# Performance work log

Hardware: AMD Instinct MI355X
Metric: run time of the kernel (lower is better)

The kernel has to match this reference:

```python
import jax, jax.numpy as jnp
import numpy as np

B, S, H, NH = 8, 512, 4096, 64
HD = H // NH  # head dim = 64
LN_EPS = 1e-12
TOL_BITS = 16


def quant16(x):
    """Per-tensor dynamic fixed-point quantization to 16 bits.

    int_bit_width = ceil(log2(max|x|)) + 1 (sign bit); frac = 16 - int_bits.
    Values are rounded to the fixed-point grid and clipped to int16 range.
    """
    m = jnp.max(jnp.abs(x))
    int_bw = jnp.ceil(jnp.log2(jnp.maximum(m, 1e-12))) + 1.0
    frac_bw = jnp.asarray(TOL_BITS, x.dtype) - int_bw
    scale = jnp.exp2(frac_bw).astype(x.dtype)
    q = jnp.clip(jnp.round(x * scale), -32768.0, 32767.0) / scale
    return q


def setup_inputs() -> dict:
    key = jax.random.key(0)
    ks = jax.random.split(key, 6)
    s = 0.02
    return {
        "input_ids": jax.random.normal(ks[0], (B, S, H), jnp.float32),
        "attention_mask": jnp.zeros((B, 1, 1, S), jnp.float32),
        "Wq": jax.random.normal(ks[1], (H, H), jnp.float32) * s,
        "bq": jnp.zeros((H,), jnp.float32),
        "Wk": jax.random.normal(ks[2], (H, H), jnp.float32) * s,
        "bk": jnp.zeros((H,), jnp.float32),
        "Wv": jax.random.normal(ks[3], (H, H), jnp.float32) * s,
        "bv": jnp.zeros((H,), jnp.float32),
        "Wd": jax.random.normal(ks[4], (H, H), jnp.float32) * s,
        "bd": jnp.zeros((H,), jnp.float32),
        "ln_w": jnp.ones((H,), jnp.float32),
        "ln_b": jnp.zeros((H,), jnp.float32),
    }


def reference(input_ids, attention_mask, Wq, bq, Wk, bk, Wv, bv, Wd, bd, ln_w, ln_b):
    x = input_ids  # [B,S,H]
    # Q/K/V projections (torch Linear: y = x @ W.T + b), each followed by quant
    q = quant16(jnp.einsum('bsh,oh->bso', x, Wq) + bq)
    k = quant16(jnp.einsum('bsh,oh->bso', x, Wk) + bk)
    v = quant16(jnp.einsum('bsh,oh->bso', x, Wv) + bv)
    # split heads -> [B,NH,S,HD]
    q = q.reshape(B, S, NH, HD).transpose(0, 2, 1, 3)
    k = k.reshape(B, S, NH, HD).transpose(0, 2, 1, 3)
    v = v.reshape(B, S, NH, HD).transpose(0, 2, 1, 3)
    scores = jnp.einsum('bnqd,bnkd->bnqk', q, k) / np.sqrt(HD).astype(np.float32)
    scores = quant16(scores)
    scores = scores + attention_mask
    probs = jax.nn.softmax(scores, axis=-1)
    probs = quant16(probs)
    ctx = quant16(jnp.einsum('bnqk,bnkd->bnqd', probs, v))
    ctx = ctx.transpose(0, 2, 1, 3)  # [B,S,NH,HD]
    # dense: w = Wd.T reshaped to (NH, HD, H)
    w = Wd.T.reshape(NH, HD, H)
    proj = quant16(jnp.einsum('bfnd,ndh->bfh', ctx, w) + bd)
    # residual + LayerNorm
    y = x + proj
    mu = jnp.mean(y, axis=-1, keepdims=True)
    var = jnp.mean(jnp.square(y - mu), axis=-1, keepdims=True)
    y = (y - mu) / jnp.sqrt(var + LN_EPS) * ln_w + ln_b
    return quant16(y)
```

## Files before the change

kernel.cpp:

```cpp
#include <hip/hip_runtime.h>
#include <hip/hip_bf16.h>
#include <stdint.h>


typedef __attribute__((ext_vector_type(4))) float f32x4;
typedef __attribute__((ext_vector_type(8))) __bf16 bf16x8;

__device__ inline unsigned short f2bf(float f) {
  union { float f; unsigned u; } c; c.f = f;
  unsigned r = (c.u + 0x7fffu + ((c.u >> 16) & 1u)) >> 16;
  return (unsigned short)r;
}

__device__ inline void gload_lds16(const void* g, void* l) {
  __builtin_amdgcn_global_load_lds(
      (const __attribute__((address_space(1))) void*)g,
      (__attribute__((address_space(3))) void*)l, 16, 0, 0);
}

__global__ __launch_bounds__(256) void conv_all(
    const float* __restrict__ x, const float* __restrict__ wq,
    const float* __restrict__ wk, const float* __restrict__ wv,
    const float* __restrict__ wd, unsigned short* __restrict__ out) {
  int i = blockIdx.x * 256 + threadIdx.x;
  int reg = i >> 21;
  int off = i & 2097151;
  const float* src = (reg == 0) ? x : (reg == 1) ? wq : (reg == 2) ? wk
                     : (reg == 3) ? wv : wd;
  const float4* ip = (const float4*)src;
  float4 a = ip[off * 2], b = ip[off * 2 + 1];
  union { unsigned short s[8]; uint4 v; } o;
  o.s[0] = f2bf(a.x); o.s[1] = f2bf(a.y); o.s[2] = f2bf(a.z); o.s[3] = f2bf(a.w);
  o.s[4] = f2bf(b.x); o.s[5] = f2bf(b.y); o.s[6] = f2bf(b.z); o.s[7] = f2bf(b.w);
  ((uint4*)out)[i] = o.v;
}

template <int BIAS_MODE, int OUT_BF16>
__global__ __launch_bounds__(512, 2) void gemm_4p(
    const unsigned short* __restrict__ A, const unsigned short* __restrict__ Bw,
    const float* __restrict__ bias0, const float* __restrict__ bias1,
    const float* __restrict__ bias2, void* __restrict__ Cout,
    int M, int N, int K) {
  extern __shared__ unsigned short lds[];
  const int nbm = M >> 8, nbn = N >> 8, nwg = nbm * nbn;
  const int bid = blockIdx.x;
  const int wg = (bid & 7) * (nwg >> 3) + (bid >> 3);
  const int bm = wg % nbm, bn = wg / nbm;
  const int tid = threadIdx.x, w = tid >> 6, l = tid & 63;
  const int wr = w >> 2, wc = w & 3;
  const int lr = l & 15, lg = l >> 4;
  const unsigned short* gA = A + (size_t)bm * 256 * K;
  const unsigned short* gB = Bw + (size_t)bn * 256 * K;
  const int NT = K >> 6;
  const int srow = tid >> 3;
  const int scol = ((tid & 7) ^ (srow & 7)) << 3;
  f32x4 acc[8][4] = {};
  bf16x8 a[8], b[8];

#define STG(op, buf, h, kt)                                                    \
  {                                                                            \
    const unsigned short* g_ = (op) ? gB : gA;                                 \
    _Pragma("unroll")                                                          \
    for (int j_ = 0; j_ < 2; ++j_) {                                           \
      gload_lds16(                                                             \
          g_ + (size_t)((h) * 128 + j_ * 64 + srow) * K + (kt) * 64 + scol,    \
          &lds[((op) * 2 + (buf)) * 16384 + ((h) * 128 + j_ * 64) * 64 +       \
               w * 512]);                                                      \
    }                                                                          \
  }

#define RDA(buf, m, kk)                                                        \
  (*(const bf16x8*)&lds[(buf) * 16384 + (wr * 128 + (m) * 16 + lr) * 64 +      \
                        ((((kk) * 4 + lg) ^ (lr & 7)) << 3)])
#define RDB(buf, n, kk)                                                        \
  (*(const bf16x8*)&lds[(2 + (buf)) * 16384 + (wc * 64 + (n) * 16 + lr) * 64 + \
                        ((((kk) * 4 + lg) ^ (lr & 7)) << 3)])

#define LDA(buf, mh)                                                           \
  _Pragma("unroll")                                                            \
  for (int m_ = 0; m_ < 4; ++m_) {                                             \
    a[m_ * 2 + 0] = RDA(buf, (mh) * 4 + m_, 0);                                \
    a[m_ * 2 + 1] = RDA(buf, (mh) * 4 + m_, 1);                                \
  }
#define LDB(buf, nh)                                                           \
  _Pragma("unroll")                                                            \
  for (int n_ = 0; n_ < 2; ++n_) {                                             \
    b[((nh) * 2 + n_) * 2 + 0] = RDB(buf, (nh) * 2 + n_, 0);                   \
    b[((nh) * 2 + n_) * 2 + 1] = RDB(buf, (nh) * 2 + n_, 1);                   \
  }

#define MM(mbase, nbase)                                                       \
  __builtin_amdgcn_s_setprio(1);                                               \
  _Pragma("unroll")                                                            \
  for (int m_ = 0; m_ < 4; ++m_) {                                             \
    _Pragma("unroll")                                                          \
    for (int n_ = 0; n_ < 2; ++n_) {                                           \
      acc[(mbase) + m_][(nbase) + n_] =                                        \
          __builtin_amdgcn_mfma_f32_16x16x32_bf16(                             \
              a[m_ * 2], b[((nbase) + n_) * 2], acc[(mbase) + m_][(nbase) + n_],\
              0, 0, 0);                                                        \
      acc[(mbase) + m_][(nbase) + n_] =                                        \
          __builtin_amdgcn_mfma_f32_16x16x32_bf16(                             \
              a[m_ * 2 + 1], b[((nbase) + n_) * 2 + 1],                        \
              acc[(mbase) + m_][(nbase) + n_], 0, 0, 0);                       \
    }                                                                          \
  }                                                                            \
  __builtin_amdgcn_s_setprio(0);

#define BAR() __builtin_amdgcn_s_barrier()
#define VMW4() asm volatile("s_waitcnt vmcnt(4)" ::: "memory")
#define VMW0() asm volatile("s_waitcnt vmcnt(0)" ::: "memory")

  STG(0, 0, 0, 0); STG(0, 0, 1, 0); STG(1, 0, 0, 0); STG(1, 0, 1, 0);
  STG(1, 1, 0, 1); STG(1, 1, 1, 1);
  VMW4();
  BAR();

  const int NI = NT >> 1;
  for (int i = 0; i < NI; ++i) {
    const int t1 = 2 * i + 1, t2 = 2 * i + 2, t3 = 2 * i + 3;
    const bool s2 = t2 < NT, s3 = t3 < NT;
    LDA(0, 0); LDB(0, 0); LDB(0, 1);
    STG(0, 1, 0, t1); STG(0, 1, 1, t1);
    BAR();
    MM(0, 0); MM(0, 2);
    LDA(0, 1);
    if (s2) { STG(1, 0, 0, t2); STG(1, 0, 1, t2); VMW4(); } else VMW0();
    BAR();
    MM(4, 0); MM(4, 2);
    LDA(1, 0); LDB(1, 0); LDB(1, 1);
    if (s2) { STG(0, 0, 0, t2); STG(0, 0, 1, t2); }
    BAR();
    MM(0, 0); MM(0, 2);
    LDA(1, 1);
    if (s3) { STG(1, 1, 0, t3); STG(1, 1, 1, t3); VMW4(); }
    else if (s2) VMW0();
    BAR();
    MM(4, 0); MM(4, 2);
  }

#pragma unroll
  for (int n = 0; n < 4; ++n) {
    int col = bn * 256 + wc * 64 + n * 16 + lr;
    float bv = 0.f;
    if (BIAS_MODE == 1) bv = bias0[col];
    else if (BIAS_MODE == 2)
      bv = (col < 4096) ? bias0[col] : (col < 8192 ? bias1[col - 4096] : bias2[col - 8192]);
#pragma unroll
    for (int m = 0; m < 8; ++m) {
#pragma unroll
      for (int r = 0; r < 4; ++r) {
        int row = bm * 256 + wr * 128 + m * 16 + lg * 4 + r;
        float v = acc[m][n][r] + bv;
        if (OUT_BF16)
          ((unsigned short*)Cout)[(size_t)row * N + col] = f2bf(v);
        else
          ((float*)Cout)[(size_t)row * N + col] = v;
      }
    }
  }
#undef STG
#undef RDA
#undef RDB
#undef LDA
#undef LDB
#undef MM
#undef BAR
#undef VMW4
#undef VMW0
}

__global__ __launch_bounds__(512) void attn_kernel(
    const unsigned short* __restrict__ qkv, const float* __restrict__ mask,
    unsigned short* __restrict__ ctx) {
  extern __shared__ char smem[];
  unsigned short* Kt = (unsigned short*)smem;
  unsigned short* Vt = Kt + 512 * 64;
  unsigned short* Pb = Vt + 64 * 512;
  float* Mb = (float*)(Pb + 8 * 16 * 64);

  const int bid = blockIdx.x;
  const int b = bid >> 6, h = bid & 63;
  const int tid = threadIdx.x, w = tid >> 6, l = tid & 63;
  const size_t tokbase = (size_t)b * 512;

  Mb[tid < 512 ? tid : 0] = mask[b * 512 + (tid < 512 ? tid : 0)];
#pragma unroll
  for (int it = 0; it < 8; ++it) {
    int idx = it * 512 + tid;
    int row = idx >> 3, g = (idx & 7) << 3;
    const unsigned short* src = qkv + (tokbase + row) * 12288 + 4096 + h * 64 + g;
    uint4 v = *(const uint4*)src;
    *(uint4*)&Kt[row * 64 + (g ^ ((row & 7) << 3))] = v;
  }
#pragma unroll
  for (int it = 0; it < 8; ++it) {
    int idx = it * 512 + tid;
    int key = idx >> 3, g = (idx & 7) << 3;
    const unsigned short* src = qkv + (tokbase + key) * 12288 + 8192 + h * 64 + g;
    uint4 v = *(const uint4*)src;
    const unsigned short* e = (const unsigned short*)&v;
#pragma unroll
    for (int i = 0; i < 8; i++) {
      int d = g + i;
      Vt[d * 512 + (key ^ ((d & 7) << 3))] = e[i];
    }
  }
  __syncthreads();

  unsigned short* Pw = Pb + w * 16 * 64;
  const int lr = l & 15, lg = l >> 4;

  for (int c = 0; c < 4; ++c) {
    int q0 = w * 64 + c * 16;
    const unsigned short* qsrc = qkv + (tokbase + q0 + lr) * 12288 + h * 64 + lg * 8;
    bf16x8 qa0 = *(const bf16x8*)qsrc;
    bf16x8 qa1 = *(const bf16x8*)(qsrc + 32);
    f32x4 sc[32];
    f32x4 zero = {0.f, 0.f, 0.f, 0.f};
#pragma unroll
    for (int n = 0; n < 32; n++) {
      int key = n * 16 + lr;
      bf16x8 kb0 = *(const bf16x8*)&Kt[key * 64 + ((lg * 8) ^ ((key & 7) << 3))];
      bf16x8 kb1 = *(const bf16x8*)&Kt[key * 64 + ((32 + lg * 8) ^ ((key & 7) << 3))];
      f32x4 a = __builtin_amdgcn_mfma_f32_16x16x32_bf16(qa0, kb0, zero, 0, 0, 0);
      sc[n] = __builtin_amdgcn_mfma_f32_16x16x32_bf16(qa1, kb1, a, 0, 0, 0);
    }
    float rmax[4] = {-1e30f, -1e30f, -1e30f, -1e30f};
#pragma unroll
    for (int n = 0; n < 32; n++) {
      float mk = Mb[n * 16 + lr];
#pragma unroll
      for (int r = 0; r < 4; r++) {
        float s = sc[n][r] * 0.125f + mk;
        sc[n][r] = s;
        rmax[r] = fmaxf(rmax[r], s);
      }
    }
#pragma unroll
    for (int r = 0; r < 4; r++) {
      float m = rmax[r];
      m = fmaxf(m, __shfl_xor(m, 8)); m = fmaxf(m, __shfl_xor(m, 4));
      m = fmaxf(m, __shfl_xor(m, 2)); m = fmaxf(m, __shfl_xor(m, 1));
      rmax[r] = m;
    }
    float rsum[4] = {0.f, 0.f, 0.f, 0.f};
#pragma unroll
    for (int n = 0; n < 32; n++)
#pragma unroll
      for (int r = 0; r < 4; r++) {
        float p = __expf(sc[n][r] - rmax[r]);
        sc[n][r] = p;
        rsum[r] += p;
      }
#pragma unroll
    for (int r = 0; r < 4; r++) {
      float s = rsum[r];
      s += __shfl_xor(s, 8); s += __shfl_xor(s, 4);
      s += __shfl_xor(s, 2); s += __shfl_xor(s, 1);
      rsum[r] = s;
    }
    f32x4 cacc[4] = {};
#pragma unroll
    for (int kb = 0; kb < 8; ++kb) {
#pragma unroll
      for (int nn = 0; nn < 4; ++nn) {
        int colp = nn * 16 + lr;
#pragma unroll
        for (int r = 0; r < 4; r++) {
          int m = lg * 4 + r;
          Pw[m * 64 + (colp ^ ((m & 7) << 3))] = f2bf(sc[kb * 4 + nn][r]);
        }
      }
      bf16x8 pa0 = *(const bf16x8*)&Pw[lr * 64 + ((lg * 8) ^ ((lr & 7) << 3))];
      bf16x8 pa1 = *(const bf16x8*)&Pw[lr * 64 + ((32 + lg * 8) ^ ((lr & 7) << 3))];
#pragma unroll
      for (int dt = 0; dt < 4; ++dt) {
        int vr = dt * 16 + lr;
        int k0 = kb * 64 + lg * 8;
        bf16x8 vb0 = *(const bf16x8*)&Vt[vr * 512 + (k0 ^ ((vr & 7) << 3))];
        bf16x8 vb1 = *(const bf16x8*)&Vt[vr * 512 + ((k0 + 32) ^ ((vr & 7) << 3))];
        cacc[dt] = __builtin_amdgcn_mfma_f32_16x16x32_bf16(pa0, vb0, cacc[dt], 0, 0, 0);
        cacc[dt] = __builtin_amdgcn_mfma_f32_16x16x32_bf16(pa1, vb1, cacc[dt], 0, 0, 0);
      }
    }
#pragma unroll
    for (int dt = 0; dt < 4; ++dt)
#pragma unroll
      for (int r = 0; r < 4; r++) {
        int row = q0 + lg * 4 + r;
        float v = cacc[dt][r] / rsum[r];
        ctx[(tokbase + row) * 4096 + h * 64 + dt * 16 + lr] = f2bf(v);
      }
  }
}

__global__ __launch_bounds__(256) void ln_kernel(
    const float* __restrict__ x, float* __restrict__ io,
    const float* __restrict__ lnw, const float* __restrict__ lnb) {
  int t = blockIdx.x;
  const float4* xr = (const float4*)(x + (size_t)t * 4096);
  float4* pr = (float4*)(io + (size_t)t * 4096);
  float4 y[4];
  float sum = 0.f, sq = 0.f;
#pragma unroll
  for (int j = 0; j < 4; j++) {
    int i4 = j * 256 + threadIdx.x;
    float4 xv = xr[i4], pv = pr[i4];
    float4 yy;
    yy.x = xv.x + pv.x; yy.y = xv.y + pv.y; yy.z = xv.z + pv.z; yy.w = xv.w + pv.w;
    sum += yy.x + yy.y + yy.z + yy.w;
    sq += yy.x * yy.x + yy.y * yy.y + yy.z * yy.z + yy.w * yy.w;
    y[j] = yy;
  }
#pragma unroll
  for (int off = 32; off >= 1; off >>= 1) {
    sum += __shfl_down(sum, off);
    sq += __shfl_down(sq, off);
  }
  __shared__ float red[8];
  int w = threadIdx.x >> 6, l = threadIdx.x & 63;
  if (l == 0) { red[w] = sum; red[4 + w] = sq; }
  __syncthreads();
  float ts = red[0] + red[1] + red[2] + red[3];
  float tq = red[4] + red[5] + red[6] + red[7];
  float mean = ts * (1.f / 4096.f);
  float var = tq * (1.f / 4096.f) - mean * mean;
  float rs = rsqrtf(var + 1e-12f);
#pragma unroll
  for (int j = 0; j < 4; j++) {
    int i4 = j * 256 + threadIdx.x;
    float4 wv = ((const float4*)lnw)[i4];
    float4 bb = ((const float4*)lnb)[i4];
    float4 o;
    o.x = (y[j].x - mean) * rs * wv.x + bb.x;
    o.y = (y[j].y - mean) * rs * wv.y + bb.y;
    o.z = (y[j].z - mean) * rs * wv.z + bb.z;
    o.w = (y[j].w - mean) * rs * wv.w + bb.w;
    pr[i4] = o;
  }
}

extern "C" void kernel_launch(void* const* d_in, const int* in_sizes, int n_in,
                              void* d_out, int out_size, void* d_ws, size_t ws_size,
                              hipStream_t stream) {
  const float* x   = (const float*)d_in[0];
  const float* msk = (const float*)d_in[1];
  const float* Wq  = (const float*)d_in[2];
  const float* bq  = (const float*)d_in[3];
  const float* Wk  = (const float*)d_in[4];
  const float* bk  = (const float*)d_in[5];
  const float* Wv  = (const float*)d_in[6];
  const float* bv  = (const float*)d_in[7];
  const float* Wd  = (const float*)d_in[8];
  const float* bd  = (const float*)d_in[9];
  const float* lnw = (const float*)d_in[10];
  const float* lnb = (const float*)d_in[11];
  float* out = (float*)d_out;

  unsigned short* xb    = (unsigned short*)d_ws;
  unsigned short* wqkvb = xb + (size_t)16777216;
  unsigned short* wdb   = wqkvb + (size_t)50331648;
  unsigned short* qkvb  = wdb + (size_t)16777216;
  unsigned short* ctxb  = wqkvb;

  conv_all<<<40960, 256, 0, stream>>>(x, Wq, Wk, Wv, Wd, xb);

  (void)hipFuncSetAttribute((const void*)(gemm_4p<2, 1>),
                            hipFuncAttributeMaxDynamicSharedMemorySize, 131072);
  (void)hipFuncSetAttribute((const void*)(gemm_4p<1, 0>),
                            hipFuncAttributeMaxDynamicSharedMemorySize, 131072);

  gemm_4p<2, 1><<<768, 512, 131072, stream>>>(xb, wqkvb, bq, bk, bv, qkvb,
                                              4096, 12288, 4096);

  (void)hipFuncSetAttribute((const void*)attn_kernel,
                            hipFuncAttributeMaxDynamicSharedMemorySize, 149504);
  attn_kernel<<<512, 512, 149504, stream>>>(qkvb, msk, ctxb);

  gemm_4p<1, 0><<<256, 512, 131072, stream>>>(ctxb, wdb, bd, nullptr, nullptr,
                                              out, 4096, 4096, 4096);

  ln_kernel<<<4096, 256, 0, stream>>>(x, out, lnw, lnb);
}
```

Before: 740.6 us.

## Shrink GEMM tiles to 128x128 with 4 waves per workgroup

The bf16 GEMM now uses 128x128 output tiles computed by 256 threads (4 waves in a 2x2 grid), where before it used 256x256 tiles with 512 threads. LDS per block drops from 128KB to 64KB and the grids grow to 3072 and 1024 workgroups. The aim is better wave coverage across the CUs, most of all for the output-projection GEMM, which before launched only 256 blocks. The cost is lower arithmetic intensity per tile and more global and L2 traffic, since each operand tile is reloaded more often.

New measurement: 864.3 us. 16.7% more time.

```diff
diff --git a/kernel.cpp b/kernel.cpp
--- a/kernel.cpp
+++ b/kernel.cpp
@@ -36,26 +36,26 @@
 }
 
 template <int BIAS_MODE, int OUT_BF16>
-__global__ __launch_bounds__(512, 2) void gemm_4p(
+__global__ __launch_bounds__(256, 2) void gemm_4p(
     const unsigned short* __restrict__ A, const unsigned short* __restrict__ Bw,
     const float* __restrict__ bias0, const float* __restrict__ bias1,
     const float* __restrict__ bias2, void* __restrict__ Cout,
     int M, int N, int K) {
   extern __shared__ unsigned short lds[];
-  const int nbm = M >> 8, nbn = N >> 8, nwg = nbm * nbn;
+  const int nbm = M >> 7, nbn = N >> 7, nwg = nbm * nbn;
   const int bid = blockIdx.x;
   const int wg = (bid & 7) * (nwg >> 3) + (bid >> 3);
   const int bm = wg % nbm, bn = wg / nbm;
   const int tid = threadIdx.x, w = tid >> 6, l = tid & 63;
-  const int wr = w >> 2, wc = w & 3;
+  const int wr = w >> 1, wc = w & 1;
   const int lr = l & 15, lg = l >> 4;
-  const unsigned short* gA = A + (size_t)bm * 256 * K;
-  const unsigned short* gB = Bw + (size_t)bn * 256 * K;
+  const unsigned short* gA = A + (size_t)bm * 128 * K;
+  const unsigned short* gB = Bw + (size_t)bn * 128 * K;
   const int NT = K >> 6;
   const int srow = tid >> 3;
   const int scol = ((tid & 7) ^ (srow & 7)) << 3;
-  f32x4 acc[8][4] = {};
-  bf16x8 a[8], b[8];
+  f32x4 acc[4][4] = {};
+  bf16x8 a[4], b[8];
 
 #define STG(op, buf, h, kt)                                                    \
   {                                                                            \
@@ -63,46 +63,42 @@
     _Pragma("unroll")                                                          \
     for (int j_ = 0; j_ < 2; ++j_) {                                           \
       gload_lds16(                                                             \
-          g_ + (size_t)((h) * 128 + j_ * 64 + srow) * K + (kt) * 64 + scol,    \
-          &lds[((op) * 2 + (buf)) * 16384 + ((h) * 128 + j_ * 64) * 64 +       \
-               w * 512]);                                                      \
+          g_ + (size_t)((h) * 64 + j_ * 32 + srow) * K + (kt) * 64 + scol,     \
+          &lds[((op) * 2 + (buf)) * 8192 + ((h) * 64 + j_ * 32) * 64 +         \
+               tid * 8]);                                                      \
     }                                                                          \
   }
 
 #define RDA(buf, m, kk)                                                        \
-  (*(const bf16x8*)&lds[(buf) * 16384 + (wr * 128 + (m) * 16 + lr) * 64 +      \
+  (*(const bf16x8*)&lds[(buf) * 8192 + (wr * 64 + (m) * 16 + lr) * 64 +        \
                         ((((kk) * 4 + lg) ^ (lr & 7)) << 3)])
 #define RDB(buf, n, kk)                                                        \
-  (*(const bf16x8*)&lds[(2 + (buf)) * 16384 + (wc * 64 + (n) * 16 + lr) * 64 + \
+  (*(const bf16x8*)&lds[(2 + (buf)) * 8192 + (wc * 64 + (n) * 16 + lr) * 64 +  \
                         ((((kk) * 4 + lg) ^ (lr & 7)) << 3)])
 
 #define LDA(buf, mh)                                                           \
   _Pragma("unroll")                                                            \
-  for (int m_ = 0; m_ < 4; ++m_) {                                             \
-    a[m_ * 2 + 0] = RDA(buf, (mh) * 4 + m_, 0);                                \
-    a[m_ * 2 + 1] = RDA(buf, (mh) * 4 + m_, 1);                                \
-  }
-#define LDB(buf, nh)                                                           \
+  for (int m_ = 0; m_ < 2; ++m_) {                                             \
+    a[m_ * 2 + 0] = RDA(buf, (mh) * 2 + m_, 0);                                \
+    a[m_ * 2 + 1] = RDA(buf, (mh) * 2 + m_, 1);                                \
+  }
+#define LDB(buf)                                                               \
   _Pragma("unroll")                                                            \
-  for (int n_ = 0; n_ < 2; ++n_) {                                             \
-    b[((nh) * 2 + n_) * 2 + 0] = RDB(buf, (nh) * 2 + n_, 0);                   \
-    b[((nh) * 2 + n_) * 2 + 1] = RDB(buf, (nh) * 2 + n_, 1);                   \
-  }
-
-#define MM(mbase, nbase)                                                       \
+  for (int n_ = 0; n_ < 4; ++n_) {                                             \
+    b[n_ * 2 + 0] = RDB(buf, n_, 0);                                           \
+    b[n_ * 2 + 1] = RDB(buf, n_, 1);                                           \
+  }
+
+#define MM(mbase)                                                              \
   __builtin_amdgcn_s_setprio(1);                                               \
   _Pragma("unroll")                                                            \
-  for (int m_ = 0; m_ < 4; ++m_) {                                             \
+  for (int m_ = 0; m_ < 2; ++m_) {                                             \
     _Pragma("unroll")                                                          \
-    for (int n_ = 0; n_ < 2; ++n_) {                                           \
-      acc[(mbase) + m_][(nbase) + n_] =                                        \
-          __builtin_amdgcn_mfma_f32_16x16x32_bf16(                             \
-              a[m_ * 2], b[((nbase) + n_) * 2], acc[(mbase) + m_][(nbase) + n_],\
-              0, 0, 0);                                                        \
-      acc[(mbase) + m_][(nbase) + n_] =                                        \
-          __builtin_amdgcn_mfma_f32_16x16x32_bf16(                             \
-              a[m_ * 2 + 1], b[((nbase) + n_) * 2 + 1],                        \
-              acc[(mbase) + m_][(nbase) + n_], 0, 0, 0);                       \
+    for (int n_ = 0; n_ < 4; ++n_) {                                           \
+      acc[(mbase) + m_][n_] = __builtin_amdgcn_mfma_f32_16x16x32_bf16(         \
+          a[m_ * 2], b[n_ * 2], acc[(mbase) + m_][n_], 0, 0, 0);               \
+      acc[(mbase) + m_][n_] = __builtin_amdgcn_mfma_f32_16x16x32_bf16(         \
+          a[m_ * 2 + 1], b[n_ * 2 + 1], acc[(mbase) + m_][n_], 0, 0, 0);       \
     }                                                                          \
   }                                                                            \
   __builtin_amdgcn_s_setprio(0);
@@ -120,37 +116,37 @@
   for (int i = 0; i < NI; ++i) {
     const int t1 = 2 * i + 1, t2 = 2 * i + 2, t3 = 2 * i + 3;
     const bool s2 = t2 < NT, s3 = t3 < NT;
-    LDA(0, 0); LDB(0, 0); LDB(0, 1);
+    LDA(0, 0); LDB(0);
     STG(0, 1, 0, t1); STG(0, 1, 1, t1);
     BAR();
-    MM(0, 0); MM(0, 2);
+    MM(0);
     LDA(0, 1);
     if (s2) { STG(1, 0, 0, t2); STG(1, 0, 1, t2); VMW4(); } else VMW0();
     BAR();
-    MM(4, 0); MM(4, 2);
-    LDA(1, 0); LDB(1, 0); LDB(1, 1);
+    MM(2);
+    LDA(1, 0); LDB(1);
     if (s2) { STG(0, 0, 0, t2); STG(0, 0, 1, t2); }
     BAR();
-    MM(0, 0); MM(0, 2);
+    MM(0);
     LDA(1, 1);
     if (s3) { STG(1, 1, 0, t3); STG(1, 1, 1, t3); VMW4(); }
     else if (s2) VMW0();
     BAR();
-    MM(4, 0); MM(4, 2);
+    MM(2);
   }
 
 #pragma unroll
   for (int n = 0; n < 4; ++n) {
-    int col = bn * 256 + wc * 64 + n * 16 + lr;
+    int col = bn * 128 + wc * 64 + n * 16 + lr;
     float bv = 0.f;
     if (BIAS_MODE == 1) bv = bias0[col];
     else if (BIAS_MODE == 2)
       bv = (col < 4096) ? bias0[col] : (col < 8192 ? bias1[col - 4096] : bias2[col - 8192]);
 #pragma unroll
-    for (int m = 0; m < 8; ++m) {
+    for (int m = 0; m < 4; ++m) {
 #pragma unroll
       for (int r = 0; r < 4; ++r) {
-        int row = bm * 256 + wr * 128 + m * 16 + lg * 4 + r;
+        int row = bm * 128 + wr * 64 + m * 16 + lg * 4 + r;
         float v = acc[m][n][r] + bv;
         if (OUT_BF16)
           ((unsigned short*)Cout)[(size_t)row * N + col] = f2bf(v);
@@ -367,18 +363,18 @@
   conv_all<<<40960, 256, 0, stream>>>(x, Wq, Wk, Wv, Wd, xb);
 
   (void)hipFuncSetAttribute((const void*)(gemm_4p<2, 1>),
-                            hipFuncAttributeMaxDynamicSharedMemorySize, 131072);
+                            hipFuncAttributeMaxDynamicSharedMemorySize, 65536);
   (void)hipFuncSetAttribute((const void*)(gemm_4p<1, 0>),
-                            hipFuncAttributeMaxDynamicSharedMemorySize, 131072);
-
-  gemm_4p<2, 1><<<768, 512, 131072, stream>>>(xb, wqkvb, bq, bk, bv, qkvb,
+                            hipFuncAttributeMaxDynamicSharedMemorySize, 65536);
+
+  gemm_4p<2, 1><<<3072, 256, 65536, stream>>>(xb, wqkvb, bq, bk, bv, qkvb,
                                               4096, 12288, 4096);
 
   (void)hipFuncSetAttribute((const void*)attn_kernel,
                             hipFuncAttributeMaxDynamicSharedMemorySize, 149504);
   attn_kernel<<<512, 512, 149504, stream>>>(qkvb, msk, ctxb);
 
-  gemm_4p<1, 0><<<256, 512, 131072, stream>>>(ctxb, wdb, bd, nullptr, nullptr,
+  gemm_4p<1, 0><<<1024, 256, 65536, stream>>>(ctxb, wdb, bd, nullptr, nullptr,
                                               out, 4096, 4096, 4096);
 
   ln_kernel<<<4096, 256, 0, stream>>>(x, out, lnw, lnb);
```
